# Performance work log

Measured on AMD Instinct MI355X. Metric: run time of the kernel, lower is better.

The kernel has to match this reference:

```python
import jax, jax.numpy as jnp
import numpy as np

N_NODES = 50000
N_EDGES = 640000
F_IN = 64
EDGE_DIM = 16
HID = 128
N_LAYERS = 3
N_CLASSES = 2
NUM_GRAPHS = 64
BN_EPS = 1e-5


def setup_inputs() -> dict:
    key = jax.random.key(0)
    ks = jax.random.split(key, 20)
    s = 0.05
    inp = {
        "x": jax.random.normal(ks[0], (N_NODES, F_IN), dtype=jnp.float32),
        "edge_index": jax.random.randint(ks[1], (2, N_EDGES), 0, N_NODES, dtype=jnp.int32),
        "edge_attr": jax.random.normal(ks[2], (N_EDGES, EDGE_DIM), dtype=jnp.float32),
        "batch": jnp.sort(jax.random.randint(ks[3], (N_NODES,), 0, NUM_GRAPHS, dtype=jnp.int32)),
        # node encoder
        "enc_W": jax.random.normal(ks[4], (F_IN, HID), dtype=jnp.float32) * s,
        "enc_b": jnp.zeros((HID,), dtype=jnp.float32),
        # per-layer GINEConv params (stacked over layers)
        "edge_W": jax.random.normal(ks[5], (N_LAYERS, EDGE_DIM, HID), dtype=jnp.float32) * s,
        "edge_b": jnp.zeros((N_LAYERS, HID), dtype=jnp.float32),
        "mlp_W1": jax.random.normal(ks[6], (N_LAYERS, HID, HID), dtype=jnp.float32) * s,
        "mlp_b1": jnp.zeros((N_LAYERS, HID), dtype=jnp.float32),
        "mlp_W2": jax.random.normal(ks[7], (N_LAYERS, HID, HID), dtype=jnp.float32) * s,
        "mlp_b2": jnp.zeros((N_LAYERS, HID), dtype=jnp.float32),
        "bn_gamma": jnp.ones((N_LAYERS, HID), dtype=jnp.float32),
        "bn_beta": jnp.zeros((N_LAYERS, HID), dtype=jnp.float32),
        # classification head
        "head_W1": jax.random.normal(ks[8], (HID, HID), dtype=jnp.float32) * s,
        "head_b1": jnp.zeros((HID,), dtype=jnp.float32),
        "head_W2": jax.random.normal(ks[9], (HID, N_CLASSES), dtype=jnp.float32) * s,
        "head_b2": jnp.zeros((N_CLASSES,), dtype=jnp.float32),
    }
    return inp


def reference(x, edge_index, edge_attr, batch, enc_W, enc_b, edge_W, edge_b,
              mlp_W1, mlp_b1, mlp_W2, mlp_b2, bn_gamma, bn_beta,
              head_W1, head_b1, head_W2, head_b2):
    src, dst = edge_index[0], edge_index[1]  # message flows src -> dst
    h = x @ enc_W + enc_b  # [N, HID]
    for l in range(N_LAYERS):
        # GINEConv: msg = ReLU(x_src + Lin(edge_attr)); aggr = scatter_add at dst
        e = edge_attr @ edge_W[l] + edge_b[l]          # [E, HID]
        msg = jax.nn.relu(h[src] + e)                  # [E, HID]
        agg = jax.ops.segment_sum(msg, dst, num_segments=N_NODES)
        z = h + agg  # (1 + eps) * x + aggr, eps = 0
        # node MLP: Linear-ReLU-Linear
        z = jax.nn.relu(z @ mlp_W1[l] + mlp_b1[l]) @ mlp_W2[l] + mlp_b2[l]
        # BatchNorm1d (training-mode batch stats) + ReLU (dropout = identity)
        mean = jnp.mean(z, axis=0)
        var = jnp.var(z, axis=0)
        z = bn_gamma[l] * (z - mean) * jax.lax.rsqrt(var + BN_EPS) + bn_beta[l]
        h = jax.nn.relu(z)
    # global_add_pool over graphs
    g = jax.ops.segment_sum(h, batch, num_segments=NUM_GRAPHS)  # [G, HID]
    out = jax.nn.relu(g @ head_W1 + head_b1) @ head_W2 + head_b2
    return out  # [G, N_CLASSES]
```

## Files before the change

### kernel.cpp

```cpp
#include <hip/hip_runtime.h>
#include <hip/hip_bf16.h>

#define N_NODES 50000
#define N_EDGES 640000
#define F_IN 64
#define EDGE_DIM 16
#define HID 128
#define N_LAYERS 3
#define NUM_GRAPHS 64
#define BN_EPS 1e-5f

typedef __attribute__((ext_vector_type(8))) short short8;
typedef __attribute__((ext_vector_type(4))) float f32x4;
typedef __attribute__((ext_vector_type(2))) __fp16 half2v;
typedef __attribute__((ext_vector_type(8))) __fp16 half8;

__device__ __forceinline__ float bfl(unsigned int u) {
    unsigned int v = u << 16; float f; __builtin_memcpy(&f, &v, 4); return f;
}
__device__ __forceinline__ float bfh(unsigned int u) {
    unsigned int v = u & 0xffff0000u; float f; __builtin_memcpy(&f, &v, 4); return f;
}
__device__ __forceinline__ unsigned int f2bf(float f) {
    unsigned int v; __builtin_memcpy(&v, &f, 4);
    v += 0x7fffu + ((v >> 16) & 1u);
    return v >> 16;
}
__device__ __forceinline__ unsigned int pack2(float lo, float hi) {
    return f2bf(lo) | (f2bf(hi) << 16);
}
__device__ __forceinline__ unsigned int pkh(float a, float b) {
    half2v h = __builtin_amdgcn_cvt_pkrtz(a, b);
    unsigned int u; __builtin_memcpy(&u, &h, 4); return u;
}

__global__ void k_hist(const int* __restrict__ dst, int* __restrict__ deg) {
    int e = blockIdx.x * 256 + threadIdx.x;
    atomicAdd(&deg[dst[e]], 1);
}

__global__ void k_blockred(const int* __restrict__ deg, int* __restrict__ bsums) {
    __shared__ int s[256];
    int i = blockIdx.x * 256 + threadIdx.x;
    int v = (i < N_NODES) ? deg[i] : 0;
    s[threadIdx.x] = v;
    __syncthreads();
    for (int off = 128; off > 0; off >>= 1) {
        if (threadIdx.x < off) s[threadIdx.x] += s[threadIdx.x + off];
        __syncthreads();
    }
    if (threadIdx.x == 0) bsums[blockIdx.x] = s[0];
}

__global__ void k_scan_bsums(int* __restrict__ bsums, int nb) {
    __shared__ int s[256];
    const int tid = threadIdx.x;
    const int v = (tid < nb) ? bsums[tid] : 0;
    s[tid] = v;
    __syncthreads();
    for (int off = 1; off < 256; off <<= 1) {
        int t = 0;
        if (tid >= off) t = s[tid - off];
        __syncthreads();
        s[tid] += t;
        __syncthreads();
    }
    if (tid < nb) bsums[tid] = s[tid] - v;
}

__global__ void k_scan_blocks(int* __restrict__ deg_rowptr, const int* __restrict__ bsums,
                              int* __restrict__ cursor) {
    __shared__ int s[256];
    int tid = threadIdx.x;
    int i = blockIdx.x * 256 + tid;
    int v = (i < N_NODES) ? deg_rowptr[i] : 0;
    s[tid] = v;
    __syncthreads();
    for (int off = 1; off < 256; off <<= 1) {
        int t = 0;
        if (tid >= off) t = s[tid - off];
        __syncthreads();
        s[tid] += t;
        __syncthreads();
    }
    int excl = s[tid] - v + bsums[blockIdx.x];
    if (i < N_NODES) {
        deg_rowptr[i] = excl;
        cursor[i] = excl;
    }
    if (i == N_NODES - 1) deg_rowptr[N_NODES] = N_EDGES;
}

__global__ void k_fill(const int* __restrict__ dst, int* __restrict__ cursor,
                       int* __restrict__ elist) {
    int e = blockIdx.x * 256 + threadIdx.x;
    int p = atomicAdd(&cursor[dst[e]], 1);
    elist[p] = e;
}

__global__ __launch_bounds__(256) void k_gather(const int* __restrict__ elist,
                                                const int* __restrict__ esrc,
                                                const float* __restrict__ eattr,
                                                int* __restrict__ src_s,
                                                uint4* __restrict__ eattr_h) {
    const int base = blockIdx.x * 1024;
    const int tid = threadIdx.x;
    int p[4], eid[4];
#pragma unroll
    for (int j = 0; j < 4; ++j) p[j] = base + tid + j * 256;
#pragma unroll
    for (int j = 0; j < 4; ++j) eid[j] = elist[p[j]];
    int sv[4];
#pragma unroll
    for (int j = 0; j < 4; ++j) sv[j] = esrc[eid[j]];
    float4 a[4][4];
#pragma unroll
    for (int j = 0; j < 4; ++j) {
        const float* ep = eattr + (size_t)eid[j] * EDGE_DIM;
        a[j][0] = *(const float4*)ep;
        a[j][1] = *(const float4*)(ep + 4);
        a[j][2] = *(const float4*)(ep + 8);
        a[j][3] = *(const float4*)(ep + 12);
    }
#pragma unroll
    for (int j = 0; j < 4; ++j) {
        src_s[p[j]] = sv[j];
        eattr_h[p[j] * 2] = make_uint4(pkh(a[j][0].x, a[j][0].y), pkh(a[j][0].z, a[j][0].w),
                                       pkh(a[j][1].x, a[j][1].y), pkh(a[j][1].z, a[j][1].w));
        eattr_h[p[j] * 2 + 1] = make_uint4(pkh(a[j][2].x, a[j][2].y), pkh(a[j][2].z, a[j][2].w),
                                           pkh(a[j][3].x, a[j][3].y), pkh(a[j][3].z, a[j][3].w));
    }
}

__global__ void k_pack(const float* __restrict__ W1, const float* __restrict__ W2,
                       const float* __restrict__ encW, const float* __restrict__ eW,
                       const float* __restrict__ eb2,
                       unsigned short* __restrict__ wp, unsigned short* __restrict__ wpe,
                       unsigned short* __restrict__ wekf) {
    const int t = blockIdx.x * 256 + threadIdx.x;
    if (t < 12288) {
        const int mat = t >> 11;
        const int r = t & 2047;
        const int kstep = r >> 9;
        const int ntile = (r >> 6) & 7;
        const int lane = r & 63;
        const float* W = (mat < 3) ? (W1 + mat * 16384) : (W2 + (mat - 3) * 16384);
        const int kbase = kstep * 32 + ((lane >> 4) << 3);
        const int n = ntile * 16 + (lane & 15);
        unsigned int o[4];
#pragma unroll
        for (int jj = 0; jj < 4; ++jj)
            o[jj] = pack2(W[(kbase + 2 * jj) * HID + n], W[(kbase + 2 * jj + 1) * HID + n]);
        *(uint4*)(wp + (size_t)mat * 16384 + (((kstep << 3) + ntile) * 64 + lane) * 8) =
            make_uint4(o[0], o[1], o[2], o[3]);
    } else if (t < 13312) {
        const int r = t - 12288;
        const int kstep = r >> 9;
        const int ntile = (r >> 6) & 7;
        const int lane = r & 63;
        const int kbase = kstep * 32 + ((lane >> 4) << 3);
        const int n = ntile * 16 + (lane & 15);
        unsigned int o[4];
#pragma unroll
        for (int jj = 0; jj < 4; ++jj)
            o[jj] = pack2(encW[(kbase + 2 * jj) * HID + n], encW[(kbase + 2 * jj + 1) * HID + n]);
        *(uint4*)(wpe + (((kstep << 3) + ntile) * 64 + lane) * 8) =
            make_uint4(o[0], o[1], o[2], o[3]);
    } else {
        const int r = t - 13312;
        const int l = r >> 10;
        const int rr = r & 1023;
        const int nt = rr >> 7;
        const int lane = (rr >> 1) & 63;
        const int hf = rr & 1;
        const int qq = lane >> 4;
        const int f = ((lane & 15) << 3) + nt;
        float v[4];
#pragma unroll
        for (int j = 0; j < 4; ++j) {
            const int k = (qq << 3) + (hf << 2) + j;
            v[j] = (k < 16) ? eW[(l * EDGE_DIM + k) * HID + f]
                            : ((k == 16) ? eb2[l * HID + f] : 0.f);
        }
        *(uint2*)(wekf + (((l * 8 + nt) * 64 + lane) * 8) + (hf << 2)) =
            make_uint2(pkh(v[0], v[1]), pkh(v[2], v[3]));
    }
}

__global__ __launch_bounds__(256, 3) void k_encm(const float* __restrict__ x,
                                                 const unsigned short* __restrict__ wpe,
                                                 const float* __restrict__ b,
                                                 unsigned short* __restrict__ hb) {
    const int tid = threadIdx.x;
    const int w = tid >> 6, lane = tid & 63;
    const int q = lane >> 4, l15 = lane & 15;
    const int row0 = blockIdx.x * 64 + w * 16;
    const int ar = min(row0 + l15, N_NODES - 1);
    const float* xp = x + (size_t)ar * F_IN + q * 8;
    f32x4 acc[8];
#pragma unroll
    for (int nt = 0; nt < 8; ++nt) acc[nt] = (f32x4){0.f, 0.f, 0.f, 0.f};
#pragma unroll
    for (int ks = 0; ks < 2; ++ks) {
        const float4 v0 = *(const float4*)(xp + ks * 32);
        const float4 v1 = *(const float4*)(xp + ks * 32 + 4);
        unsigned int u[4] = {pack2(v0.x, v0.y), pack2(v0.z, v0.w),
                             pack2(v1.x, v1.y), pack2(v1.z, v1.w)};
        short8 a; __builtin_memcpy(&a, u, 16);
#pragma unroll
        for (int nt = 0; nt < 8; ++nt) {
            const short8 bf = *(const short8*)(wpe + (((ks << 3) + nt) * 64 + lane) * 8);
            acc[nt] = __builtin_amdgcn_mfma_f32_16x16x32_bf16(a, bf, acc[nt], 0, 0, 0);
        }
    }
    const int rowb = row0 + q * 4;
#pragma unroll
    for (int nt = 0; nt < 8; ++nt) {
        const float bias = b[nt * 16 + l15];
        const int cc = nt * 16 + l15;
#pragma unroll
        for (int reg = 0; reg < 4; ++reg) {
            const int r = rowb + reg;
            if (r < N_NODES)
                hb[(size_t)r * HID + cc] = (unsigned short)f2bf(acc[nt][reg] + bias);
        }
    }
}

__global__ __launch_bounds__(256) void k_bn(const unsigned short* __restrict__ z,
                                            const float* __restrict__ bnst,
                                            const float* __restrict__ gamma,
                                            const float* __restrict__ beta,
                                            unsigned short* __restrict__ hb2) {
    const int idx = blockIdx.x * 256 + threadIdx.x;
    const int f0 = (idx * 8) & 127;
    const float invN = 1.0f / (float)N_NODES;
    uint4 v = *(const uint4*)(z + (size_t)idx * 8);
    const unsigned int* u = (const unsigned int*)&v;
    unsigned int o[4];
#pragma unroll
    for (int p = 0; p < 4; ++p) {
        const int f = f0 + 2 * p;
        const float m0 = bnst[f] * invN;
        const float m1 = bnst[f + 1] * invN;
        const float v0 = fmaxf(bnst[128 + f] * invN - m0 * m0, 0.f);
        const float v1 = fmaxf(bnst[128 + f + 1] * invN - m1 * m1, 0.f);
        const float r0 = rsqrtf(v0 + BN_EPS), r1 = rsqrtf(v1 + BN_EPS);
        const float sc0 = gamma[f] * r0, sc1 = gamma[f + 1] * r1;
        const float sh0 = fmaf(-m0, sc0, beta[f]);
        const float sh1 = fmaf(-m1, sc1, beta[f + 1]);
        const float a = fmaxf(fmaf(bfl(u[p]), sc0, sh0), 0.f);
        const float b = fmaxf(fmaf(bfh(u[p]), sc1, sh1), 0.f);
        o[p] = pack2(a, b);
    }
    *(uint4*)(hb2 + (size_t)idx * 8) = make_uint4(o[0], o[1], o[2], o[3]);
}

__global__ __launch_bounds__(256, 2) void k_agg(const unsigned short* __restrict__ hrow,
                                                const int* __restrict__ src_s,
                                                const uint4* __restrict__ eattr_h,
                                                const unsigned short* __restrict__ wekf,
                                                const int* __restrict__ row_ptr,
                                                unsigned int* __restrict__ zb32) {
    const int lane = threadIdx.x & 63;
    const int wv = threadIdx.x >> 6;
    const int q = lane >> 4, l15 = lane & 15;
    const int f0 = l15 * 8;

    half8 Bf[8];
#pragma unroll
    for (int nt = 0; nt < 8; ++nt) {
        uint4 u = *(const uint4*)(wekf + (nt * 64 + lane) * 8);
        __builtin_memcpy(&Bf[nt], &u, 16);
    }

    const int n = blockIdx.x * 4 + wv;
    const int base = __builtin_amdgcn_readfirstlane(row_ptr[n]);
    const int deg  = __builtin_amdgcn_readfirstlane(row_ptr[n + 1]) - base;

    float accf[8];
#pragma unroll
    for (int j = 0; j < 8; ++j) accf[j] = 0.f;

    if (deg > 0) {
        const int ntile = (deg + 15) >> 4;
        for (int t = 0; t < ntile; ++t) {
            const int e0 = t * 16;
            uint4 au = make_uint4(0u, 0u, 0u, 0u);
            if (q < 2) {
                const int ea = min(e0 + l15, deg - 1);
                au = eattr_h[(size_t)(base + ea) * 2 + q];
            } else if (q == 2) {
                au.x = 0x3C00u;
            }
            half8 Af; __builtin_memcpy(&Af, &au, 16);

            int sv[4];
#pragma unroll
            for (int r = 0; r < 4; ++r)
                sv[r] = src_s[base + min(e0 + q * 4 + r, deg - 1)];
            uint4 hg[4];
#pragma unroll
            for (int r = 0; r < 4; ++r)
                hg[r] = *(const uint4*)(hrow + (size_t)sv[r] * HID + f0);

            f32x4 acc[8];
#pragma unroll
            for (int nt = 0; nt < 8; ++nt) {
                acc[nt] = (f32x4){0.f, 0.f, 0.f, 0.f};
                acc[nt] = __builtin_amdgcn_mfma_f32_16x16x32_f16(Af, Bf[nt], acc[nt], 0, 0, 0);
            }

#pragma unroll
            for (int r = 0; r < 4; ++r) {
                const float m = (e0 + q * 4 + r < deg) ? 1.f : 0.f;
                const unsigned int* hu = (const unsigned int*)&hg[r];
#pragma unroll
                for (int p = 0; p < 4; ++p) {
                    accf[2 * p]     = fmaf(m, fmaxf(bfl(hu[p]) + acc[2 * p][r],     0.f), accf[2 * p]);
                    accf[2 * p + 1] = fmaf(m, fmaxf(bfh(hu[p]) + acc[2 * p + 1][r], 0.f), accf[2 * p + 1]);
                }
            }
        }
    }

#pragma unroll
    for (int j = 0; j < 8; ++j) {
        accf[j] += __shfl_xor(accf[j], 16, 64);
        accf[j] += __shfl_xor(accf[j], 32, 64);
    }

    if (q == 0) {
        const uint4 hs = *(const uint4*)(hrow + (size_t)n * HID + f0);
        const unsigned int* hu = (const unsigned int*)&hs;
        unsigned int o[4];
#pragma unroll
        for (int p = 0; p < 4; ++p)
            o[p] = pack2(bfl(hu[p]) + accf[2 * p], bfh(hu[p]) + accf[2 * p + 1]);
        *(uint4*)(zb32 + (size_t)n * 64 + l15 * 4) = make_uint4(o[0], o[1], o[2], o[3]);
    }
}

#define Z1LD 136

__global__ __launch_bounds__(256, 3) void k_mlp(const unsigned short* __restrict__ zb,
                                                const unsigned short* __restrict__ w1p,
                                                const float* __restrict__ b1,
                                                const unsigned short* __restrict__ w2p,
                                                const float* __restrict__ b2,
                                                unsigned short* __restrict__ z2b,
                                                float* __restrict__ bn) {
    __shared__ unsigned short z1s[64 * Z1LD];
    __shared__ float redA[512];
    __shared__ float redB[512];
    const int tid = threadIdx.x;
    const int w = tid >> 6, lane = tid & 63;
    const int q = lane >> 4, l15 = lane & 15;
    const int row0 = blockIdx.x * 64 + w * 16;

    const int ar = min(row0 + l15, N_NODES - 1);
    const unsigned short* aptr = zb + (size_t)ar * HID + q * 8;

    f32x4 acc[8];
#pragma unroll
    for (int nt = 0; nt < 8; ++nt) acc[nt] = (f32x4){0.f, 0.f, 0.f, 0.f};

#pragma unroll
    for (int ks = 0; ks < 4; ++ks) {
        const short8 a = *(const short8*)(aptr + ks * 32);
#pragma unroll
        for (int nt = 0; nt < 8; ++nt) {
            const short8 b = *(const short8*)(w1p + (((ks << 3) + nt) * 64 + lane) * 8);
            acc[nt] = __builtin_amdgcn_mfma_f32_16x16x32_bf16(a, b, acc[nt], 0, 0, 0);
        }
    }
    {
        const int lr0 = w * 16 + q * 4;
#pragma unroll
        for (int nt = 0; nt < 8; ++nt) {
            const float bias = b1[nt * 16 + l15];
            const int cc = nt * 16 + l15;
#pragma unroll
            for (int reg = 0; reg < 4; ++reg) {
                const float v = fmaxf(acc[nt][reg] + bias, 0.f);
                z1s[(lr0 + reg) * Z1LD + cc] = (unsigned short)f2bf(v);
            }
        }
    }
#pragma unroll
    for (int nt = 0; nt < 8; ++nt) acc[nt] = (f32x4){0.f, 0.f, 0.f, 0.f};
    const unsigned short* a2p = &z1s[(w * 16 + l15) * Z1LD + q * 8];
#pragma unroll
    for (int ks = 0; ks < 4; ++ks) {
        const short8 a = *(const short8*)(a2p + ks * 32);
#pragma unroll
        for (int nt = 0; nt < 8; ++nt) {
            const short8 b = *(const short8*)(w2p + (((ks << 3) + nt) * 64 + lane) * 8);
            acc[nt] = __builtin_amdgcn_mfma_f32_16x16x32_bf16(a, b, acc[nt], 0, 0, 0);
        }
    }
    float s[8], sq[8];
    const int rowb = row0 + q * 4;
#pragma unroll
    for (int nt = 0; nt < 8; ++nt) {
        const float bias = b2[nt * 16 + l15];
        const int cc = nt * 16 + l15;
        float ls = 0.f, lq = 0.f;
#pragma unroll
        for (int reg = 0; reg < 4; ++reg) {
            const int r = rowb + reg;
            const float v = acc[nt][reg] + bias;
            if (r < N_NODES) {
                z2b[(size_t)r * HID + cc] = (unsigned short)f2bf(v);
                ls += v;
                lq = fmaf(v, v, lq);
            }
        }
        s[nt] = ls; sq[nt] = lq;
    }
#pragma unroll
    for (int nt = 0; nt < 8; ++nt) {
        s[nt] += __shfl_xor(s[nt], 16, 64);
        s[nt] += __shfl_xor(s[nt], 32, 64);
        sq[nt] += __shfl_xor(sq[nt], 16, 64);
        sq[nt] += __shfl_xor(sq[nt], 32, 64);
    }
    if (lane < 16) {
#pragma unroll
        for (int nt = 0; nt < 8; ++nt) {
            redA[w * 128 + nt * 16 + lane] = s[nt];
            redB[w * 128 + nt * 16 + lane] = sq[nt];
        }
    }
    __syncthreads();
    if (tid < 128) {
        float t = redA[tid] + redA[128 + tid] + redA[256 + tid] + redA[384 + tid];
        atomicAdd(&bn[tid], t);
    } else {
        const int c = tid - 128;
        float t = redB[c] + redB[128 + c] + redB[256 + c] + redB[384 + c];
        atomicAdd(&bn[128 + c], t);
    }
}

__global__ void k_pool(const unsigned short* __restrict__ z2b, const int* __restrict__ batch,
                       const float* __restrict__ bnst, const float* __restrict__ gamma,
                       const float* __restrict__ beta, float* __restrict__ g) {
    const int f = threadIdx.x;
    const float invN = 1.0f / (float)N_NODES;
    const float m = bnst[f] * invN;
    const float var = fmaxf(bnst[128 + f] * invN - m * m, 0.f);
    const float r = rsqrtf(var + BN_EPS);
    const float sc = gamma[f] * r;
    const float sh = fmaf(-m, sc, beta[f]);

    const int n0 = blockIdx.x * 128;
    const int nend = min(n0 + 128, N_NODES);
    float acc = 0.f;
    int cur = batch[n0];
    for (int n = n0; n < nend; ++n) {
        const int bb = batch[n];
        if (bb != cur) {
            atomicAdd(&g[cur * HID + f], acc);
            acc = 0.f;
            cur = bb;
        }
        const float raw = bfl((unsigned int)z2b[n * HID + f]);
        acc += fmaxf(fmaf(raw, sc, sh), 0.f);
    }
    atomicAdd(&g[cur * HID + f], acc);
}

__global__ void k_head1(const float* __restrict__ g, const float* __restrict__ W,
                        const float* __restrict__ b, float* __restrict__ g1) {
    const int idx = blockIdx.x * 256 + threadIdx.x;
    const int r = idx >> 7, c = idx & 127;
    float acc = b[c];
    for (int k = 0; k < 128; ++k) acc = fmaf(g[r * HID + k], W[k * HID + c], acc);
    g1[idx] = fmaxf(acc, 0.f);
}

__global__ void k_head2(const float* __restrict__ g1, const float* __restrict__ W,
                        const float* __restrict__ b, float* __restrict__ out) {
    const int idx = threadIdx.x;
    const int r = idx >> 1, c = idx & 1;
    float acc = b[c];
    for (int k = 0; k < 128; ++k) acc = fmaf(g1[r * HID + k], W[k * 2 + c], acc);
    out[idx] = acc;
}

extern "C" void kernel_launch(void* const* d_in, const int* in_sizes, int n_in,
                              void* d_out, int out_size, void* d_ws, size_t ws_size,
                              hipStream_t stream) {
    const float* x     = (const float*)d_in[0];
    const int*   ei    = (const int*)d_in[1];
    const float* eattr = (const float*)d_in[2];
    const int*   batch = (const int*)d_in[3];
    const float* encW  = (const float*)d_in[4];
    const float* encb  = (const float*)d_in[5];
    const float* eW    = (const float*)d_in[6];
    const float* eb    = (const float*)d_in[7];
    const float* W1    = (const float*)d_in[8];
    const float* b1    = (const float*)d_in[9];
    const float* W2    = (const float*)d_in[10];
    const float* b2    = (const float*)d_in[11];
    const float* gam   = (const float*)d_in[12];
    const float* bet   = (const float*)d_in[13];
    const float* hW1   = (const float*)d_in[14];
    const float* hb1   = (const float*)d_in[15];
    const float* hW2   = (const float*)d_in[16];
    const float* hb2w  = (const float*)d_in[17];
    float* out = (float*)d_out;

    float* ws = (float*)d_ws;
    unsigned short* z2b = (unsigned short*)ws;
    float* bn  = ws + 3200000;
    float* g   = ws + 3200256;
    float* g1  = ws + 3208448;
    unsigned short* hb  = (unsigned short*)(ws + 3216640);
    unsigned int* zb32  = (unsigned int*)(ws + 6416640);
    unsigned short* hb2 = (unsigned short*)(ws + 9616640);
    unsigned short* wekf = (unsigned short*)(ws + 12816640);
    unsigned short* wp  = (unsigned short*)(ws + 12822784);
    unsigned short* wpe = (unsigned short*)(ws + 12871936);
    int* row_ptr = (int*)(ws + 12876032);
    int* cursor  = row_ptr + N_NODES + 1;
    int* elist   = cursor + N_NODES;
    int* bsums   = elist + N_EDGES;
    int* src_s   = bsums + 256;
    uint4* eattr_h = (uint4*)(ws + 14256292);

    const int* esrc = ei;
    const int* edst = ei + N_EDGES;

    hipMemsetAsync(row_ptr, 0, (N_NODES + 1) * sizeof(int), stream);
    k_hist<<<N_EDGES / 256, 256, 0, stream>>>(edst, row_ptr);
    k_blockred<<<196, 256, 0, stream>>>(row_ptr, bsums);
    k_scan_bsums<<<1, 256, 0, stream>>>(bsums, 196);
    k_scan_blocks<<<196, 256, 0, stream>>>(row_ptr, bsums, cursor);
    k_fill<<<N_EDGES / 256, 256, 0, stream>>>(edst, cursor, elist);
    k_gather<<<N_EDGES / 1024, 256, 0, stream>>>(elist, esrc, eattr, src_s, eattr_h);

    k_pack<<<64, 256, 0, stream>>>(W1, W2, encW, eW, eb, wp, wpe, wekf);

    k_encm<<<782, 256, 0, stream>>>(x, wpe, encb, hb);

    for (int l = 0; l < N_LAYERS; ++l) {
        const unsigned short* hrow;
        if (l == 0) {
            hrow = hb;
        } else {
            k_bn<<<3125, 256, 0, stream>>>(z2b, bn, gam + (l - 1) * HID,
                                           bet + (l - 1) * HID, hb2);
            hrow = hb2;
        }
        k_agg<<<12500, 256, 0, stream>>>(hrow, src_s, eattr_h,
                                         wekf + (size_t)l * 4096, row_ptr, zb32);
        hipMemsetAsync(bn, 0, 256 * sizeof(float), stream);
        k_mlp<<<782, 256, 0, stream>>>((const unsigned short*)zb32,
                                       wp + (size_t)l * 16384, b1 + l * HID,
                                       wp + (size_t)(3 + l) * 16384, b2 + l * HID,
                                       z2b, bn);
    }

    hipMemsetAsync(g, 0, NUM_GRAPHS * HID * sizeof(float), stream);
    k_pool<<<391, 128, 0, stream>>>(z2b, batch, bn, gam + 2 * HID, bet + 2 * HID, g);
    k_head1<<<32, 256, 0, stream>>>(g, hW1, hb1, g1);
    k_head2<<<1, 128, 0, stream>>>(g1, hW2, hb2w, out);
}
```

Baseline: 533.2 us.

## Process two nodes per wave in aggregation with hoisted first-tile gathers

Each wavefront in the aggregation kernel now handles two destination nodes. All index, edge-attribute and neighbour-row loads for the first 16-edge tile of both nodes are issued up front, before the MFMA and accumulate work, and any later tiles go through a helper loop. The aim is more memory-level parallelism for the latency-bound gather, since the average degree is about 13 and most nodes fit in one tile. The cost is higher register pressure, and the launch bound drops its occupancy hint.

```diff
diff --git a/kernel.cpp b/kernel.cpp
--- a/kernel.cpp
+++ b/kernel.cpp
@@ -256,17 +256,81 @@
     *(uint4*)(hb2 + (size_t)idx * 8) = make_uint4(o[0], o[1], o[2], o[3]);
 }
 
-__global__ __launch_bounds__(256, 2) void k_agg(const unsigned short* __restrict__ hrow,
-                                                const int* __restrict__ src_s,
-                                                const uint4* __restrict__ eattr_h,
-                                                const unsigned short* __restrict__ wekf,
-                                                const int* __restrict__ row_ptr,
-                                                unsigned int* __restrict__ zb32) {
+__device__ __forceinline__ void agg_tail(const unsigned short* __restrict__ hrow,
+                                         const int* __restrict__ sp,
+                                         const uint4* __restrict__ ep,
+                                         const half8* Bf, int deg,
+                                         int q, int l15, int f0, float* accf) {
+    const int ntile = (deg + 15) >> 4;
+    for (int t = 1; t < ntile; ++t) {
+        const int e0 = t * 16;
+        uint4 au = make_uint4(0u, 0u, 0u, 0u);
+        if (q < 2) au = ep[(size_t)min(e0 + l15, deg - 1) * 2 + q];
+        else if (q == 2) au.x = 0x3C00u;
+        half8 Af; __builtin_memcpy(&Af, &au, 16);
+        int sv[4];
+#pragma unroll
+        for (int r = 0; r < 4; ++r) sv[r] = sp[min(e0 + q * 4 + r, deg - 1)];
+        uint4 hg[4];
+#pragma unroll
+        for (int r = 0; r < 4; ++r)
+            hg[r] = *(const uint4*)(hrow + (size_t)sv[r] * HID + f0);
+        f32x4 acc[8];
+#pragma unroll
+        for (int nt = 0; nt < 8; ++nt) {
+            acc[nt] = (f32x4){0.f, 0.f, 0.f, 0.f};
+            acc[nt] = __builtin_amdgcn_mfma_f32_16x16x32_f16(Af, Bf[nt], acc[nt], 0, 0, 0);
+        }
+#pragma unroll
+        for (int r = 0; r < 4; ++r) {
+            const float m = (e0 + q * 4 + r < deg) ? 1.f : 0.f;
+            const unsigned int* hu = (const unsigned int*)&hg[r];
+#pragma unroll
+            for (int p = 0; p < 4; ++p) {
+                accf[2 * p]     = fmaf(m, fmaxf(bfl(hu[p]) + acc[2 * p][r],     0.f), accf[2 * p]);
+                accf[2 * p + 1] = fmaf(m, fmaxf(bfh(hu[p]) + acc[2 * p + 1][r], 0.f), accf[2 * p + 1]);
+            }
+        }
+    }
+}
+
+__global__ __launch_bounds__(256) void k_agg(const unsigned short* __restrict__ hrow,
+                                             const int* __restrict__ src_s,
+                                             const uint4* __restrict__ eattr_h,
+                                             const unsigned short* __restrict__ wekf,
+                                             const int* __restrict__ row_ptr,
+                                             unsigned int* __restrict__ zb32) {
     const int lane = threadIdx.x & 63;
     const int wv = threadIdx.x >> 6;
     const int q = lane >> 4, l15 = lane & 15;
     const int f0 = l15 * 8;
 
+    const int n0 = (blockIdx.x * 4 + wv) * 2;
+
+    const int rp0 = row_ptr[n0];
+    const int rp1 = row_ptr[n0 + 1];
+    const int rp2 = row_ptr[n0 + 2];
+    const int baseA = __builtin_amdgcn_readfirstlane(rp0);
+    const int baseB = __builtin_amdgcn_readfirstlane(rp1);
+    const int endB  = __builtin_amdgcn_readfirstlane(rp2);
+    const int degA = baseB - baseA;
+    const int degB = endB - baseB;
+    const int dA1 = max(degA, 1), dB1 = max(degB, 1);
+
+    int svA[4], svB[4];
+#pragma unroll
+    for (int r = 0; r < 4; ++r) svA[r] = src_s[baseA + min(q * 4 + r, dA1 - 1)];
+#pragma unroll
+    for (int r = 0; r < 4; ++r) svB[r] = src_s[baseB + min(q * 4 + r, dB1 - 1)];
+
+    uint4 auA = make_uint4(0u, 0u, 0u, 0u), auB = make_uint4(0u, 0u, 0u, 0u);
+    if (q < 2) {
+        auA = eattr_h[(size_t)(baseA + min(l15, dA1 - 1)) * 2 + q];
+        auB = eattr_h[(size_t)(baseB + min(l15, dB1 - 1)) * 2 + q];
+    } else if (q == 2) {
+        auA.x = 0x3C00u; auB.x = 0x3C00u;
+    }
+
     half8 Bf[8];
 #pragma unroll
     for (int nt = 0; nt < 8; ++nt) {
@@ -274,70 +338,90 @@
         __builtin_memcpy(&Bf[nt], &u, 16);
     }
 
-    const int n = blockIdx.x * 4 + wv;
-    const int base = __builtin_amdgcn_readfirstlane(row_ptr[n]);
-    const int deg  = __builtin_amdgcn_readfirstlane(row_ptr[n + 1]) - base;
-
-    float accf[8];
-#pragma unroll
-    for (int j = 0; j < 8; ++j) accf[j] = 0.f;
-
-    if (deg > 0) {
-        const int ntile = (deg + 15) >> 4;
-        for (int t = 0; t < ntile; ++t) {
-            const int e0 = t * 16;
-            uint4 au = make_uint4(0u, 0u, 0u, 0u);
-            if (q < 2) {
-                const int ea = min(e0 + l15, deg - 1);
-                au = eattr_h[(size_t)(base + ea) * 2 + q];
-            } else if (q == 2) {
-                au.x = 0x3C00u;
+    uint4 hgA[4], hgB[4];
+#pragma unroll
+    for (int r = 0; r < 4; ++r) {
+        const int s = min(max(svA[r], 0), N_NODES - 1);
+        hgA[r] = *(const uint4*)(hrow + (size_t)s * HID + f0);
+    }
+#pragma unroll
+    for (int r = 0; r < 4; ++r) {
+        const int s = min(max(svB[r], 0), N_NODES - 1);
+        hgB[r] = *(const uint4*)(hrow + (size_t)s * HID + f0);
+    }
+
+    float accA[8], accB[8];
+#pragma unroll
+    for (int j = 0; j < 8; ++j) { accA[j] = 0.f; accB[j] = 0.f; }
+
+    {
+        half8 Af; __builtin_memcpy(&Af, &auA, 16);
+        f32x4 acc[8];
+#pragma unroll
+        for (int nt = 0; nt < 8; ++nt) {
+            acc[nt] = (f32x4){0.f, 0.f, 0.f, 0.f};
+            acc[nt] = __builtin_amdgcn_mfma_f32_16x16x32_f16(Af, Bf[nt], acc[nt], 0, 0, 0);
+        }
+#pragma unroll
+        for (int r = 0; r < 4; ++r) {
+            const float m = (q * 4 + r < degA) ? 1.f : 0.f;
+            const unsigned int* hu = (const unsigned int*)&hgA[r];
+#pragma unroll
+            for (int p = 0; p < 4; ++p) {
+                accA[2 * p]     = fmaf(m, fmaxf(bfl(hu[p]) + acc[2 * p][r],     0.f), accA[2 * p]);
+                accA[2 * p + 1] = fmaf(m, fmaxf(bfh(hu[p]) + acc[2 * p + 1][r], 0.f), accA[2 * p + 1]);
             }
-            half8 Af; __builtin_memcpy(&Af, &au, 16);
-
-            int sv[4];
-#pragma unroll
-            for (int r = 0; r < 4; ++r)
-                sv[r] = src_s[base + min(e0 + q * 4 + r, deg - 1)];
-            uint4 hg[4];
-#pragma unroll
-            for (int r = 0; r < 4; ++r)
-                hg[r] = *(const uint4*)(hrow + (size_t)sv[r] * HID + f0);
-
-            f32x4 acc[8];
-#pragma unroll
-            for (int nt = 0; nt < 8; ++nt) {
-                acc[nt] = (f32x4){0.f, 0.f, 0.f, 0.f};
-                acc[nt] = __builtin_amdgcn_mfma_f32_16x16x32_f16(Af, Bf[nt], acc[nt], 0, 0, 0);
+        }
+    }
+    {
+        half8 Af; __builtin_memcpy(&Af, &auB, 16);
+        f32x4 acc[8];
+#pragma unroll
+        for (int nt = 0; nt < 8; ++nt) {
+            acc[nt] = (f32x4){0.f, 0.f, 0.f, 0.f};
+            acc[nt] = __builtin_amdgcn_mfma_f32_16x16x32_f16(Af, Bf[nt], acc[nt], 0, 0, 0);
+        }
+#pragma unroll
+        for (int r = 0; r < 4; ++r) {
+            const float m = (q * 4 + r < degB) ? 1.f : 0.f;
+            const unsigned int* hu = (const unsigned int*)&hgB[r];
+#pragma unroll
+            for (int p = 0; p < 4; ++p) {
+                accB[2 * p]     = fmaf(m, fmaxf(bfl(hu[p]) + acc[2 * p][r],     0.f), accB[2 * p]);
+                accB[2 * p + 1] = fmaf(m, fmaxf(bfh(hu[p]) + acc[2 * p + 1][r], 0.f), accB[2 * p + 1]);
             }
-
-#pragma unroll
-            for (int r = 0; r < 4; ++r) {
-                const float m = (e0 + q * 4 + r < deg) ? 1.f : 0.f;
-                const unsigned int* hu = (const unsigned int*)&hg[r];
-#pragma unroll
-                for (int p = 0; p < 4; ++p) {
-                    accf[2 * p]     = fmaf(m, fmaxf(bfl(hu[p]) + acc[2 * p][r],     0.f), accf[2 * p]);
-                    accf[2 * p + 1] = fmaf(m, fmaxf(bfh(hu[p]) + acc[2 * p + 1][r], 0.f), accf[2 * p + 1]);
-                }
-            }
-        }
-    }
+        }
+    }
+
+    if (degA > 16)
+        agg_tail(hrow, src_s + baseA, eattr_h + (size_t)baseA * 2, Bf, degA, q, l15, f0, accA);
+    if (degB > 16)
+        agg_tail(hrow, src_s + baseB, eattr_h + (size_t)baseB * 2, Bf, degB, q, l15, f0, accB);
 
 #pragma unroll
     for (int j = 0; j < 8; ++j) {
-        accf[j] += __shfl_xor(accf[j], 16, 64);
-        accf[j] += __shfl_xor(accf[j], 32, 64);
+        accA[j] += __shfl_xor(accA[j], 16, 64);
+        accA[j] += __shfl_xor(accA[j], 32, 64);
+        accB[j] += __shfl_xor(accB[j], 16, 64);
+        accB[j] += __shfl_xor(accB[j], 32, 64);
     }
 
     if (q == 0) {
-        const uint4 hs = *(const uint4*)(hrow + (size_t)n * HID + f0);
+        const uint4 hs = *(const uint4*)(hrow + (size_t)n0 * HID + f0);
         const unsigned int* hu = (const unsigned int*)&hs;
         unsigned int o[4];
 #pragma unroll
         for (int p = 0; p < 4; ++p)
-            o[p] = pack2(bfl(hu[p]) + accf[2 * p], bfh(hu[p]) + accf[2 * p + 1]);
-        *(uint4*)(zb32 + (size_t)n * 64 + l15 * 4) = make_uint4(o[0], o[1], o[2], o[3]);
+            o[p] = pack2(bfl(hu[p]) + accA[2 * p], bfh(hu[p]) + accA[2 * p + 1]);
+        *(uint4*)(zb32 + (size_t)n0 * 64 + l15 * 4) = make_uint4(o[0], o[1], o[2], o[3]);
+    } else if (q == 1) {
+        const uint4 hs = *(const uint4*)(hrow + (size_t)(n0 + 1) * HID + f0);
+        const unsigned int* hu = (const unsigned int*)&hs;
+        unsigned int o[4];
+#pragma unroll
+        for (int p = 0; p < 4; ++p)
+            o[p] = pack2(bfl(hu[p]) + accB[2 * p], bfh(hu[p]) + accB[2 * p + 1]);
+        *(uint4*)(zb32 + (size_t)(n0 + 1) * 64 + l15 * 4) = make_uint4(o[0], o[1], o[2], o[3]);
     }
 }
 
@@ -554,8 +638,8 @@
                                            bet + (l - 1) * HID, hb2);
             hrow = hb2;
         }
-        k_agg<<<12500, 256, 0, stream>>>(hrow, src_s, eattr_h,
-                                         wekf + (size_t)l * 4096, row_ptr, zb32);
+        k_agg<<<6250, 256, 0, stream>>>(hrow, src_s, eattr_h,
+                                        wekf + (size_t)l * 4096, row_ptr, zb32);
         hipMemsetAsync(bn, 0, 256 * sizeof(float), stream);
         k_mlp<<<782, 256, 0, stream>>>((const unsigned short*)zb32,
                                        wp + (size_t)l * 16384, b1 + l * HID,
```

Result: slower. 568.3 us (+6.6%).

## Make edge aggregation persistent with software-prefetched next-node indices and attributes

Applied to the files above, without the earlier changes.

The aggregation kernel becomes grid-strided over nodes with a fixed grid of 2048 blocks, instead of launching one wave per node. Each wave loads its B fragments once and prefetches the next node's row pointers, source indices and edge attributes while it processes the current node. The first 16-edge tile is handled inline and any remaining edges go through a helper loop. This removes the per-wave weight reload and hides index-load latency, but it carries more registers across iterations and drops the occupancy hint from launch bounds.

```diff
diff --git a/kernel.cpp b/kernel.cpp
--- a/kernel.cpp
+++ b/kernel.cpp
@@ -256,12 +256,50 @@
     *(uint4*)(hb2 + (size_t)idx * 8) = make_uint4(o[0], o[1], o[2], o[3]);
 }
 
-__global__ __launch_bounds__(256, 2) void k_agg(const unsigned short* __restrict__ hrow,
-                                                const int* __restrict__ src_s,
-                                                const uint4* __restrict__ eattr_h,
-                                                const unsigned short* __restrict__ wekf,
-                                                const int* __restrict__ row_ptr,
-                                                unsigned int* __restrict__ zb32) {
+__device__ __forceinline__ void agg_tail(const unsigned short* __restrict__ hrow,
+                                         const int* __restrict__ sp,
+                                         const uint4* __restrict__ ep,
+                                         const half8* Bf, int deg,
+                                         int q, int l15, int f0, float* accf) {
+    const int ntile = (deg + 15) >> 4;
+    for (int t = 1; t < ntile; ++t) {
+        const int e0 = t * 16;
+        uint4 au = make_uint4(0u, 0u, 0u, 0u);
+        if (q < 2) au = ep[(size_t)min(e0 + l15, deg - 1) * 2 + q];
+        else if (q == 2) au.x = 0x3C00u;
+        half8 Af; __builtin_memcpy(&Af, &au, 16);
+        int sv[4];
+#pragma unroll
+        for (int r = 0; r < 4; ++r) sv[r] = sp[min(e0 + q * 4 + r, deg - 1)];
+        uint4 hg[4];
+#pragma unroll
+        for (int r = 0; r < 4; ++r)
+            hg[r] = *(const uint4*)(hrow + (size_t)sv[r] * HID + f0);
+        f32x4 acc[8];
+#pragma unroll
+        for (int nt = 0; nt < 8; ++nt) {
+            acc[nt] = (f32x4){0.f, 0.f, 0.f, 0.f};
+            acc[nt] = __builtin_amdgcn_mfma_f32_16x16x32_f16(Af, Bf[nt], acc[nt], 0, 0, 0);
+        }
+#pragma unroll
+        for (int r = 0; r < 4; ++r) {
+            const float m = (e0 + q * 4 + r < deg) ? 1.f : 0.f;
+            const unsigned int* hu = (const unsigned int*)&hg[r];
+#pragma unroll
+            for (int p = 0; p < 4; ++p) {
+                accf[2 * p]     = fmaf(m, fmaxf(bfl(hu[p]) + acc[2 * p][r],     0.f), accf[2 * p]);
+                accf[2 * p + 1] = fmaf(m, fmaxf(bfh(hu[p]) + acc[2 * p + 1][r], 0.f), accf[2 * p + 1]);
+            }
+        }
+    }
+}
+
+__global__ __launch_bounds__(256) void k_agg(const unsigned short* __restrict__ hrow,
+                                             const int* __restrict__ src_s,
+                                             const uint4* __restrict__ eattr_h,
+                                             const unsigned short* __restrict__ wekf,
+                                             const int* __restrict__ row_ptr,
+                                             unsigned int* __restrict__ zb32) {
     const int lane = threadIdx.x & 63;
     const int wv = threadIdx.x >> 6;
     const int q = lane >> 4, l15 = lane & 15;
@@ -274,70 +312,93 @@
         __builtin_memcpy(&Bf[nt], &u, 16);
     }
 
-    const int n = blockIdx.x * 4 + wv;
-    const int base = __builtin_amdgcn_readfirstlane(row_ptr[n]);
-    const int deg  = __builtin_amdgcn_readfirstlane(row_ptr[n + 1]) - base;
-
-    float accf[8];
-#pragma unroll
-    for (int j = 0; j < 8; ++j) accf[j] = 0.f;
-
-    if (deg > 0) {
-        const int ntile = (deg + 15) >> 4;
-        for (int t = 0; t < ntile; ++t) {
-            const int e0 = t * 16;
-            uint4 au = make_uint4(0u, 0u, 0u, 0u);
-            if (q < 2) {
-                const int ea = min(e0 + l15, deg - 1);
-                au = eattr_h[(size_t)(base + ea) * 2 + q];
-            } else if (q == 2) {
-                au.x = 0x3C00u;
+    int n = blockIdx.x * 4 + wv;
+
+    int base = __builtin_amdgcn_readfirstlane(row_ptr[n]);
+    int deg  = __builtin_amdgcn_readfirstlane(row_ptr[n + 1]) - base;
+    int d1 = max(deg, 1);
+    int sv[4];
+#pragma unroll
+    for (int r = 0; r < 4; ++r)
+        sv[r] = src_s[min(base + min(q * 4 + r, d1 - 1), N_EDGES - 1)];
+    uint4 au = make_uint4(0u, 0u, 0u, 0u);
+    if (q < 2) au = eattr_h[(size_t)min(base + min(l15, d1 - 1), N_EDGES - 1) * 2 + q];
+    else if (q == 2) au.x = 0x3C00u;
+
+    for (;;) {
+        const int nn = n + 8192;
+        const bool more = (nn < N_NODES);
+
+        int rpA = 0, rpB = 0;
+        if (more) { rpA = row_ptr[nn]; rpB = row_ptr[nn + 1]; }
+
+        uint4 hg[4];
+#pragma unroll
+        for (int r = 0; r < 4; ++r) {
+            const int s = min(max(sv[r], 0), N_NODES - 1);
+            hg[r] = *(const uint4*)(hrow + (size_t)s * HID + f0);
+        }
+
+        half8 Af; __builtin_memcpy(&Af, &au, 16);
+        f32x4 acc[8];
+#pragma unroll
+        for (int nt = 0; nt < 8; ++nt) {
+            acc[nt] = (f32x4){0.f, 0.f, 0.f, 0.f};
+            acc[nt] = __builtin_amdgcn_mfma_f32_16x16x32_f16(Af, Bf[nt], acc[nt], 0, 0, 0);
+        }
+
+        int baseN = 0, degN = 0, d1N = 1;
+        int svN[4] = {0, 0, 0, 0};
+        uint4 auN = make_uint4(0u, 0u, 0u, 0u);
+        if (more) {
+            baseN = __builtin_amdgcn_readfirstlane(rpA);
+            degN  = __builtin_amdgcn_readfirstlane(rpB) - baseN;
+            d1N = max(degN, 1);
+#pragma unroll
+            for (int r = 0; r < 4; ++r)
+                svN[r] = src_s[min(baseN + min(q * 4 + r, d1N - 1), N_EDGES - 1)];
+            if (q < 2) auN = eattr_h[(size_t)min(baseN + min(l15, d1N - 1), N_EDGES - 1) * 2 + q];
+            else if (q == 2) auN.x = 0x3C00u;
+        }
+
+        float accf[8];
+#pragma unroll
+        for (int j = 0; j < 8; ++j) accf[j] = 0.f;
+#pragma unroll
+        for (int r = 0; r < 4; ++r) {
+            const float m = (q * 4 + r < deg) ? 1.f : 0.f;
+            const unsigned int* hu = (const unsigned int*)&hg[r];
+#pragma unroll
+            for (int p = 0; p < 4; ++p) {
+                accf[2 * p]     = fmaf(m, fmaxf(bfl(hu[p]) + acc[2 * p][r],     0.f), accf[2 * p]);
+                accf[2 * p + 1] = fmaf(m, fmaxf(bfh(hu[p]) + acc[2 * p + 1][r], 0.f), accf[2 * p + 1]);
             }
-            half8 Af; __builtin_memcpy(&Af, &au, 16);
-
-            int sv[4];
-#pragma unroll
-            for (int r = 0; r < 4; ++r)
-                sv[r] = src_s[base + min(e0 + q * 4 + r, deg - 1)];
-            uint4 hg[4];
-#pragma unroll
-            for (int r = 0; r < 4; ++r)
-                hg[r] = *(const uint4*)(hrow + (size_t)sv[r] * HID + f0);
-
-            f32x4 acc[8];
-#pragma unroll
-            for (int nt = 0; nt < 8; ++nt) {
-                acc[nt] = (f32x4){0.f, 0.f, 0.f, 0.f};
-                acc[nt] = __builtin_amdgcn_mfma_f32_16x16x32_f16(Af, Bf[nt], acc[nt], 0, 0, 0);
-            }
-
-#pragma unroll
-            for (int r = 0; r < 4; ++r) {
-                const float m = (e0 + q * 4 + r < deg) ? 1.f : 0.f;
-                const unsigned int* hu = (const unsigned int*)&hg[r];
-#pragma unroll
-                for (int p = 0; p < 4; ++p) {
-                    accf[2 * p]     = fmaf(m, fmaxf(bfl(hu[p]) + acc[2 * p][r],     0.f), accf[2 * p]);
-                    accf[2 * p + 1] = fmaf(m, fmaxf(bfh(hu[p]) + acc[2 * p + 1][r], 0.f), accf[2 * p + 1]);
-                }
-            }
-        }
-    }
-
-#pragma unroll
-    for (int j = 0; j < 8; ++j) {
-        accf[j] += __shfl_xor(accf[j], 16, 64);
-        accf[j] += __shfl_xor(accf[j], 32, 64);
-    }
-
-    if (q == 0) {
-        const uint4 hs = *(const uint4*)(hrow + (size_t)n * HID + f0);
-        const unsigned int* hu = (const unsigned int*)&hs;
-        unsigned int o[4];
-#pragma unroll
-        for (int p = 0; p < 4; ++p)
-            o[p] = pack2(bfl(hu[p]) + accf[2 * p], bfh(hu[p]) + accf[2 * p + 1]);
-        *(uint4*)(zb32 + (size_t)n * 64 + l15 * 4) = make_uint4(o[0], o[1], o[2], o[3]);
+        }
+
+        if (deg > 16)
+            agg_tail(hrow, src_s + base, eattr_h + (size_t)base * 2, Bf, deg, q, l15, f0, accf);
+
+#pragma unroll
+        for (int j = 0; j < 8; ++j) {
+            accf[j] += __shfl_xor(accf[j], 16, 64);
+            accf[j] += __shfl_xor(accf[j], 32, 64);
+        }
+
+        if (q == 0) {
+            const uint4 hs = *(const uint4*)(hrow + (size_t)n * HID + f0);
+            const unsigned int* hu = (const unsigned int*)&hs;
+            unsigned int o[4];
+#pragma unroll
+            for (int p = 0; p < 4; ++p)
+                o[p] = pack2(bfl(hu[p]) + accf[2 * p], bfh(hu[p]) + accf[2 * p + 1]);
+            *(uint4*)(zb32 + (size_t)n * 64 + l15 * 4) = make_uint4(o[0], o[1], o[2], o[3]);
+        }
+
+        if (!more) break;
+        n = nn; base = baseN; deg = degN; d1 = d1N;
+#pragma unroll
+        for (int r = 0; r < 4; ++r) sv[r] = svN[r];
+        au = auN;
     }
 }
 
@@ -554,8 +615,8 @@
                                            bet + (l - 1) * HID, hb2);
             hrow = hb2;
         }
-        k_agg<<<12500, 256, 0, stream>>>(hrow, src_s, eattr_h,
-                                         wekf + (size_t)l * 4096, row_ptr, zb32);
+        k_agg<<<2048, 256, 0, stream>>>(hrow, src_s, eattr_h,
+                                        wekf + (size_t)l * 4096, row_ptr, zb32);
         hipMemsetAsync(bn, 0, 256 * sizeof(float), stream);
         k_mlp<<<782, 256, 0, stream>>>((const unsigned short*)zb32,
                                        wp + (size_t)l * 16384, b1 + l * HID,
```

New measurement: 536.3 us. No clear change (+0.6%).

## Fuse CSR fill with edge gather and make aggregation grid-stride persistent

Applied to the files above, without the earlier changes.

k_fill and k_gather are merged into a single kernel. Each edge reads its src, dst and attributes coalesced and scatters them straight to its atomically reserved CSR slot, which removes the elist indirection and one kernel launch. The aggregation kernel becomes a grid-stride loop over nodes with 2048 blocks and launch bounds raised to 8 blocks per CU, so the per-block weight-fragment loads are amortized over several nodes. The fill writes are now scattered rather than the reads, and the tighter register budget could cause spills in k_agg.

```diff
diff --git a/kernel.cpp b/kernel.cpp
--- a/kernel.cpp
+++ b/kernel.cpp
@@ -91,45 +91,26 @@
     if (i == N_NODES - 1) deg_rowptr[N_NODES] = N_EDGES;
 }
 
-__global__ void k_fill(const int* __restrict__ dst, int* __restrict__ cursor,
-                       int* __restrict__ elist) {
-    int e = blockIdx.x * 256 + threadIdx.x;
-    int p = atomicAdd(&cursor[dst[e]], 1);
-    elist[p] = e;
-}
-
-__global__ __launch_bounds__(256) void k_gather(const int* __restrict__ elist,
-                                                const int* __restrict__ esrc,
-                                                const float* __restrict__ eattr,
-                                                int* __restrict__ src_s,
-                                                uint4* __restrict__ eattr_h) {
-    const int base = blockIdx.x * 1024;
-    const int tid = threadIdx.x;
-    int p[4], eid[4];
-#pragma unroll
-    for (int j = 0; j < 4; ++j) p[j] = base + tid + j * 256;
-#pragma unroll
-    for (int j = 0; j < 4; ++j) eid[j] = elist[p[j]];
-    int sv[4];
-#pragma unroll
-    for (int j = 0; j < 4; ++j) sv[j] = esrc[eid[j]];
-    float4 a[4][4];
-#pragma unroll
-    for (int j = 0; j < 4; ++j) {
-        const float* ep = eattr + (size_t)eid[j] * EDGE_DIM;
-        a[j][0] = *(const float4*)ep;
-        a[j][1] = *(const float4*)(ep + 4);
-        a[j][2] = *(const float4*)(ep + 8);
-        a[j][3] = *(const float4*)(ep + 12);
-    }
-#pragma unroll
-    for (int j = 0; j < 4; ++j) {
-        src_s[p[j]] = sv[j];
-        eattr_h[p[j] * 2] = make_uint4(pkh(a[j][0].x, a[j][0].y), pkh(a[j][0].z, a[j][0].w),
-                                       pkh(a[j][1].x, a[j][1].y), pkh(a[j][1].z, a[j][1].w));
-        eattr_h[p[j] * 2 + 1] = make_uint4(pkh(a[j][2].x, a[j][2].y), pkh(a[j][2].z, a[j][2].w),
-                                           pkh(a[j][3].x, a[j][3].y), pkh(a[j][3].z, a[j][3].w));
-    }
+__global__ __launch_bounds__(256) void k_fill(const int* __restrict__ esrc,
+                                              const int* __restrict__ edst,
+                                              const float* __restrict__ eattr,
+                                              int* __restrict__ cursor,
+                                              int* __restrict__ src_s,
+                                              uint4* __restrict__ eattr_h) {
+    const int e = blockIdx.x * 256 + threadIdx.x;
+    const int s = esrc[e];
+    const int d = edst[e];
+    const float* ep = eattr + (size_t)e * EDGE_DIM;
+    const float4 a0 = *(const float4*)ep;
+    const float4 a1 = *(const float4*)(ep + 4);
+    const float4 a2 = *(const float4*)(ep + 8);
+    const float4 a3 = *(const float4*)(ep + 12);
+    const int p = atomicAdd(&cursor[d], 1);
+    src_s[p] = s;
+    eattr_h[p * 2] = make_uint4(pkh(a0.x, a0.y), pkh(a0.z, a0.w),
+                                pkh(a1.x, a1.y), pkh(a1.z, a1.w));
+    eattr_h[p * 2 + 1] = make_uint4(pkh(a2.x, a2.y), pkh(a2.z, a2.w),
+                                    pkh(a3.x, a3.y), pkh(a3.z, a3.w));
 }
 
 __global__ void k_pack(const float* __restrict__ W1, const float* __restrict__ W2,
@@ -256,7 +237,7 @@
     *(uint4*)(hb2 + (size_t)idx * 8) = make_uint4(o[0], o[1], o[2], o[3]);
 }
 
-__global__ __launch_bounds__(256, 2) void k_agg(const unsigned short* __restrict__ hrow,
+__global__ __launch_bounds__(256, 8) void k_agg(const unsigned short* __restrict__ hrow,
                                                 const int* __restrict__ src_s,
                                                 const uint4* __restrict__ eattr_h,
                                                 const unsigned short* __restrict__ wekf,
@@ -274,70 +255,73 @@
         __builtin_memcpy(&Bf[nt], &u, 16);
     }
 
-    const int n = blockIdx.x * 4 + wv;
-    const int base = __builtin_amdgcn_readfirstlane(row_ptr[n]);
-    const int deg  = __builtin_amdgcn_readfirstlane(row_ptr[n + 1]) - base;
-
-    float accf[8];
-#pragma unroll
-    for (int j = 0; j < 8; ++j) accf[j] = 0.f;
-
-    if (deg > 0) {
-        const int ntile = (deg + 15) >> 4;
-        for (int t = 0; t < ntile; ++t) {
-            const int e0 = t * 16;
-            uint4 au = make_uint4(0u, 0u, 0u, 0u);
-            if (q < 2) {
-                const int ea = min(e0 + l15, deg - 1);
-                au = eattr_h[(size_t)(base + ea) * 2 + q];
-            } else if (q == 2) {
-                au.x = 0x3C00u;
-            }
-            half8 Af; __builtin_memcpy(&Af, &au, 16);
-
-            int sv[4];
-#pragma unroll
-            for (int r = 0; r < 4; ++r)
-                sv[r] = src_s[base + min(e0 + q * 4 + r, deg - 1)];
-            uint4 hg[4];
-#pragma unroll
-            for (int r = 0; r < 4; ++r)
-                hg[r] = *(const uint4*)(hrow + (size_t)sv[r] * HID + f0);
-
-            f32x4 acc[8];
-#pragma unroll
-            for (int nt = 0; nt < 8; ++nt) {
-                acc[nt] = (f32x4){0.f, 0.f, 0.f, 0.f};
-                acc[nt] = __builtin_amdgcn_mfma_f32_16x16x32_f16(Af, Bf[nt], acc[nt], 0, 0, 0);
-            }
-
-#pragma unroll
-            for (int r = 0; r < 4; ++r) {
-                const float m = (e0 + q * 4 + r < deg) ? 1.f : 0.f;
-                const unsigned int* hu = (const unsigned int*)&hg[r];
-#pragma unroll
-                for (int p = 0; p < 4; ++p) {
-                    accf[2 * p]     = fmaf(m, fmaxf(bfl(hu[p]) + acc[2 * p][r],     0.f), accf[2 * p]);
-                    accf[2 * p + 1] = fmaf(m, fmaxf(bfh(hu[p]) + acc[2 * p + 1][r], 0.f), accf[2 * p + 1]);
+    const int w0 = blockIdx.x * 4 + wv;
+
+    for (int n = w0; n < N_NODES; n += 8192) {
+        const int base = __builtin_amdgcn_readfirstlane(row_ptr[n]);
+        const int deg  = __builtin_amdgcn_readfirstlane(row_ptr[n + 1]) - base;
+
+        float accf[8];
+#pragma unroll
+        for (int j = 0; j < 8; ++j) accf[j] = 0.f;
+
+        if (deg > 0) {
+            const int ntile = (deg + 15) >> 4;
+            for (int t = 0; t < ntile; ++t) {
+                const int e0 = t * 16;
+                uint4 au = make_uint4(0u, 0u, 0u, 0u);
+                if (q < 2) {
+                    const int ea = min(e0 + l15, deg - 1);
+                    au = eattr_h[(size_t)(base + ea) * 2 + q];
+                } else if (q == 2) {
+                    au.x = 0x3C00u;
+                }
+                half8 Af; __builtin_memcpy(&Af, &au, 16);
+
+                int sv[4];
+#pragma unroll
+                for (int r = 0; r < 4; ++r)
+                    sv[r] = src_s[base + min(e0 + q * 4 + r, deg - 1)];
+                uint4 hg[4];
+#pragma unroll
+                for (int r = 0; r < 4; ++r)
+                    hg[r] = *(const uint4*)(hrow + (size_t)sv[r] * HID + f0);
+
+                f32x4 acc[8];
+#pragma unroll
+                for (int nt = 0; nt < 8; ++nt) {
+                    acc[nt] = (f32x4){0.f, 0.f, 0.f, 0.f};
+                    acc[nt] = __builtin_amdgcn_mfma_f32_16x16x32_f16(Af, Bf[nt], acc[nt], 0, 0, 0);
+                }
+
+#pragma unroll
+                for (int r = 0; r < 4; ++r) {
+                    const float m = (e0 + q * 4 + r < deg) ? 1.f : 0.f;
+                    const unsigned int* hu = (const unsigned int*)&hg[r];
+#pragma unroll
+                    for (int p = 0; p < 4; ++p) {
+                        accf[2 * p]     = fmaf(m, fmaxf(bfl(hu[p]) + acc[2 * p][r],     0.f), accf[2 * p]);
+                        accf[2 * p + 1] = fmaf(m, fmaxf(bfh(hu[p]) + acc[2 * p + 1][r], 0.f), accf[2 * p + 1]);
+                    }
                 }
             }
         }
-    }
-
-#pragma unroll
-    for (int j = 0; j < 8; ++j) {
-        accf[j] += __shfl_xor(accf[j], 16, 64);
-        accf[j] += __shfl_xor(accf[j], 32, 64);
-    }
-
-    if (q == 0) {
-        const uint4 hs = *(const uint4*)(hrow + (size_t)n * HID + f0);
-        const unsigned int* hu = (const unsigned int*)&hs;
-        unsigned int o[4];
-#pragma unroll
-        for (int p = 0; p < 4; ++p)
-            o[p] = pack2(bfl(hu[p]) + accf[2 * p], bfh(hu[p]) + accf[2 * p + 1]);
-        *(uint4*)(zb32 + (size_t)n * 64 + l15 * 4) = make_uint4(o[0], o[1], o[2], o[3]);
+
+#pragma unroll
+        for (int j = 0; j < 8; ++j) {
+            accf[j] += __shfl_xor(accf[j], 16, 64);
+            accf[j] += __shfl_xor(accf[j], 32, 64);
+        }
+
+        if (q == 0) {
+            const uint4 hs = *(const uint4*)(hrow + (size_t)n * HID + f0);
+            const unsigned int* hu = (const unsigned int*)&hs;
+            unsigned int o[4];
+#pragma unroll
+            for (int p = 0; p < 4; ++p)
+                o[p] = pack2(bfl(hu[p]) + accf[2 * p], bfh(hu[p]) + accf[2 * p + 1]);
+            *(uint4*)(zb32 + (size_t)n * 64 + l15 * 4) = make_uint4(o[0], o[1], o[2], o[3]);
+        }
     }
 }
 
@@ -538,8 +522,7 @@
     k_blockred<<<196, 256, 0, stream>>>(row_ptr, bsums);
     k_scan_bsums<<<1, 256, 0, stream>>>(bsums, 196);
     k_scan_blocks<<<196, 256, 0, stream>>>(row_ptr, bsums, cursor);
-    k_fill<<<N_EDGES / 256, 256, 0, stream>>>(edst, cursor, elist);
-    k_gather<<<N_EDGES / 1024, 256, 0, stream>>>(elist, esrc, eattr, src_s, eattr_h);
+    k_fill<<<N_EDGES / 256, 256, 0, stream>>>(esrc, edst, eattr, cursor, src_s, eattr_h);
 
     k_pack<<<64, 256, 0, stream>>>(W1, W2, encW, eW, eb, wp, wpe, wekf);
 
@@ -554,8 +537,8 @@
                                            bet + (l - 1) * HID, hb2);
             hrow = hb2;
         }
-        k_agg<<<12500, 256, 0, stream>>>(hrow, src_s, eattr_h,
-                                         wekf + (size_t)l * 4096, row_ptr, zb32);
+        k_agg<<<2048, 256, 0, stream>>>(hrow, src_s, eattr_h,
+                                        wekf + (size_t)l * 4096, row_ptr, zb32);
         hipMemsetAsync(bn, 0, 256 * sizeof(float), stream);
         k_mlp<<<782, 256, 0, stream>>>((const unsigned short*)zb32,
                                        wp + (size_t)l * 16384, b1 + l * HID,
```

Result: slower. 722.1 us (+35.4%).
